# Kernel optimization log

Measured on AMD Instinct MI355X. Metric: run time of the kernel, lower is better.

The kernel has to match this reference:

```python
import jax, jax.numpy as jnp
import numpy as np

DIM = 2048
N_HEADS = 16
HEAD_DIM = DIM // N_HEADS
ROPE_BASE = 10000


def l2norm(x, axis=-1, eps=1e-12):
    n = jnp.sqrt(jnp.sum(x * x, axis=axis, keepdims=True))
    return x / jnp.maximum(n, eps)


def rope_tables(T, dim, base, dtype):
    theta = 1.0 / (base ** (jnp.arange(0, dim, 2, dtype=dtype) / dim))  # [dim/2]
    ang = jnp.arange(T, dtype=dtype)[:, None] * theta[None, :]          # [T, dim/2]
    return jnp.sin(ang), jnp.cos(ang)


def apply_rope(x, sin, cos):
    # x: [B, H, T, D]; sin/cos: [T, D/2] (half-split convention, not interleaved)
    half = x.shape[-1] // 2
    xr, xi = x[..., :half], x[..., half:]
    yr = xr * cos - xi * sin
    yi = xr * sin + xi * cos
    return jnp.concatenate([yr, yi], axis=-1)


def setup_inputs() -> dict:
    key = jax.random.key(0)
    ks = jax.random.split(key, 5)
    B, T = 1, 2048
    x = jax.random.normal(ks[0], (B, T, DIM), dtype=jnp.float32)
    wq = jax.random.normal(ks[1], (DIM, DIM), dtype=jnp.float32) * 0.02
    wk = jax.random.normal(ks[2], (DIM, DIM), dtype=jnp.float32) * 0.02
    wv = jax.random.normal(ks[3], (DIM, DIM), dtype=jnp.float32) * 0.02
    wo = jax.random.normal(ks[4], (DIM, DIM), dtype=jnp.float32) * 0.02
    sqk = jnp.ones((N_HEADS, 1, HEAD_DIM), dtype=jnp.float32) * (1.0 / DIM ** 0.5)
    return {"x": x, "wq": wq, "wk": wk, "wv": wv, "wo": wo, "sqk": sqk}


def reference(x, wq, wk, wv, wo, sqk):
    B, T, C = x.shape
    H, D = N_HEADS, HEAD_DIM
    restore = C ** 0.5  # restore_scale_sqk = sqkinit / sqkscale
    actual_sqk = sqk * restore  # [H, 1, D]

    def proj(w):
        return jnp.einsum('btc,oc->bto', x, w).reshape(B, T, H, D).transpose(0, 2, 1, 3)

    q = proj(wq)  # [B, H, T, D]
    new_k = proj(wk)
    new_v = proj(wv)

    sin, cos = rope_tables(T, D, ROPE_BASE, x.dtype)
    q = apply_rope(q, sin, cos) * actual_sqk
    k = apply_rope(new_k, sin, cos) * actual_sqk

    # NOTE: original uses scale=head_dim**0.5 (multiplies by sqrt(D))
    scores = jnp.einsum('bhqd,bhkd->bhqk', q, k) * (D ** 0.5)
    mask = jnp.tril(jnp.ones((T, T), dtype=bool))
    scores = jnp.where(mask, scores, jnp.finfo(scores.dtype).min)
    attn = jax.nn.softmax(scores, axis=-1)
    out = jnp.einsum('bhqk,bhkd->bhqd', attn, new_v)  # [B, H, T, D]
    out = out.transpose(0, 2, 1, 3).reshape(B, T, C)
    out = jnp.einsum('btc,oc->bto', out, wo)
    return (l2norm(out), (new_k, new_v))
```

## Files before the change

### kernel.cpp

```cpp
#include <hip/hip_runtime.h>

typedef __bf16 bf16x8 __attribute__((ext_vector_type(8)));
typedef float f32x4 __attribute__((ext_vector_type(4)));
typedef unsigned short us4 __attribute__((ext_vector_type(4)));

constexpr int TT = 2048;
constexpr int CC = 2048;
constexpr int HH = 16;
constexpr int DD = 128;

__device__ __forceinline__ unsigned short f2bf(float f) {
  unsigned u = __builtin_bit_cast(unsigned, f);
  u += 0x7FFFu + ((u >> 16) & 1u);
  return (unsigned short)(u >> 16);
}
__device__ __forceinline__ float bf2f(unsigned short b) {
  unsigned u = ((unsigned)b) << 16;
  return __builtin_bit_cast(float, u);
}

__device__ __forceinline__ void gld_lds16(const unsigned short* g, unsigned short* l) {
  __builtin_amdgcn_global_load_lds(
      (const __attribute__((address_space(1))) unsigned int*)g,
      (__attribute__((address_space(3))) unsigned int*)l,
      16, 0, 0);
}

__device__ __forceinline__ int soff(int qt) {
  int g = qt >> 2, rem = qt & 3;
  return (g + 1) * (2 * g + rem);
}

__global__ __launch_bounds__(256) void k_cvt5(
    const float* __restrict__ s0, const float* __restrict__ s1,
    const float* __restrict__ s2, const float* __restrict__ s3,
    const float* __restrict__ s4,
    unsigned short* __restrict__ d0, unsigned short* __restrict__ d1,
    unsigned short* __restrict__ d2, unsigned short* __restrict__ d3,
    unsigned short* __restrict__ d4) {
  const int m = blockIdx.y;
  const float* src = (m == 0) ? s0 : (m == 1) ? s1 : (m == 2) ? s2 : (m == 3) ? s3 : s4;
  unsigned short* dst = (m == 0) ? d0 : (m == 1) ? d1 : (m == 2) ? d2 : (m == 3) ? d3 : d4;
  int i = blockIdx.x * 256 + threadIdx.x;
  const float4* s = (const float4*)src;
  float4 a = s[2 * i], b = s[2 * i + 1];
  us4 lo = { f2bf(a.x), f2bf(a.y), f2bf(a.z), f2bf(a.w) };
  us4 hi = { f2bf(b.x), f2bf(b.y), f2bf(b.z), f2bf(b.w) };
  us4* d = (us4*)dst;
  d[2 * i] = lo;
  d[2 * i + 1] = hi;
}

#define WAIT_LGKM0                                      \
  asm volatile("s_waitcnt lgkmcnt(0)" ::: "memory");    \
  __builtin_amdgcn_sched_barrier(0);
#define BAR __builtin_amdgcn_s_barrier();

__global__ __launch_bounds__(512, 2) void k_gemm192(
    const unsigned short* __restrict__ A, const unsigned short* __restrict__ B,
    unsigned short* __restrict__ qraw,
    float* __restrict__ outk, float* __restrict__ outv) {
  __shared__ alignas(16) unsigned short As[2][256 * 64];
  __shared__ alignas(16) unsigned short Bs[2][192 * 64];
  const int K = CC, NT = K >> 6, NT2 = NT >> 1;
  const int tid = threadIdx.x;
  const int m0 = blockIdx.y * 256, n0 = blockIdx.x * 192;
  const int wid = tid >> 6, lane = tid & 63;
  const int wr = wid >> 2, wc = wid & 3;
  const int lr = lane & 15, lg = lane >> 4;

  auto stA = [&](int buf, int jb, int tile) {
#pragma unroll
    for (int j = jb; j < jb + 2; ++j) {
      const int ch = tid + j * 512;
      const int r = ch >> 3, c8 = ch & 7;
      gld_lds16(A + (size_t)(m0 + r) * K + tile * 64 + ((c8 ^ (r & 7)) * 8),
                &As[buf][ch * 8]);
    }
  };
  auto stB2 = [&](int buf, int tile) {
#pragma unroll
    for (int j = 0; j < 2; ++j) {
      const int ch = tid + j * 512;
      const int r = ch >> 3, c8 = ch & 7;
      gld_lds16(B + (size_t)(n0 + r) * K + tile * 64 + ((c8 ^ (r & 7)) * 8),
                &Bs[buf][ch * 8]);
    }
  };
  auto stB1 = [&](int buf, int tile) {
    const int ch = tid + 1024;
    const int r = ch >> 3, c8 = ch & 7;
    gld_lds16(B + (size_t)(n0 + r) * K + tile * 64 + ((c8 ^ (r & 7)) * 8),
              &Bs[buf][ch * 8]);
  };

  f32x4 acc[8][3] = {};
  bf16x8 alo[4][2], ahi[4][2], b01[2][2], b2v[2];

  auto rdAlo = [&](int d) {
#pragma unroll
    for (int im = 0; im < 4; ++im)
#pragma unroll
      for (int kk = 0; kk < 2; ++kk) {
        const int row = wr * 128 + im * 16 + lr;
        alo[im][kk] = *(const bf16x8*)(&As[d][row * 64 + (((kk * 4 + lg) ^ (row & 7)) * 8)]);
      }
  };
  auto rdAhi = [&](int d) {
#pragma unroll
    for (int im = 0; im < 4; ++im)
#pragma unroll
      for (int kk = 0; kk < 2; ++kk) {
        const int row = wr * 128 + (4 + im) * 16 + lr;
        ahi[im][kk] = *(const bf16x8*)(&As[d][row * 64 + (((kk * 4 + lg) ^ (row & 7)) * 8)]);
      }
  };
  auto rdB01 = [&](int d) {
#pragma unroll
    for (int in = 0; in < 2; ++in)
#pragma unroll
      for (int kk = 0; kk < 2; ++kk) {
        const int row = wc * 48 + in * 16 + lr;
        b01[in][kk] = *(const bf16x8*)(&Bs[d][row * 64 + (((kk * 4 + lg) ^ (row & 7)) * 8)]);
      }
  };
  auto rdB2 = [&](int d) {
#pragma unroll
    for (int kk = 0; kk < 2; ++kk) {
      const int row = wc * 48 + 32 + lr;
      b2v[kk] = *(const bf16x8*)(&Bs[d][row * 64 + (((kk * 4 + lg) ^ (row & 7)) * 8)]);
    }
  };

  auto q_lo01 = [&]() {
    __builtin_amdgcn_s_setprio(1);
#pragma unroll
    for (int im = 0; im < 4; ++im)
#pragma unroll
      for (int in = 0; in < 2; ++in)
#pragma unroll
        for (int kk = 0; kk < 2; ++kk)
          acc[im][in] = __builtin_amdgcn_mfma_f32_16x16x32_bf16(alo[im][kk], b01[in][kk], acc[im][in], 0, 0, 0);
    __builtin_amdgcn_s_setprio(0);
  };
  auto q_lo2 = [&]() {
    __builtin_amdgcn_s_setprio(1);
#pragma unroll
    for (int im = 0; im < 4; ++im)
#pragma unroll
      for (int kk = 0; kk < 2; ++kk)
        acc[im][2] = __builtin_amdgcn_mfma_f32_16x16x32_bf16(alo[im][kk], b2v[kk], acc[im][2], 0, 0, 0);
    __builtin_amdgcn_s_setprio(0);
  };
  auto q_hi2 = [&]() {
    __builtin_amdgcn_s_setprio(1);
#pragma unroll
    for (int im = 0; im < 4; ++im)
#pragma unroll
      for (int kk = 0; kk < 2; ++kk)
        acc[4 + im][2] = __builtin_amdgcn_mfma_f32_16x16x32_bf16(ahi[im][kk], b2v[kk], acc[4 + im][2], 0, 0, 0);
    __builtin_amdgcn_s_setprio(0);
  };
  auto q_hi01 = [&]() {
    __builtin_amdgcn_s_setprio(1);
#pragma unroll
    for (int im = 0; im < 4; ++im)
#pragma unroll
      for (int in = 0; in < 2; ++in)
#pragma unroll
        for (int kk = 0; kk < 2; ++kk)
          acc[4 + im][in] = __builtin_amdgcn_mfma_f32_16x16x32_bf16(ahi[im][kk], b01[in][kk], acc[4 + im][in], 0, 0, 0);
    __builtin_amdgcn_s_setprio(0);
  };

  stB2(0, 0); stB1(0, 0); stA(0, 0, 0); stA(0, 2, 0);
  stB2(1, 1); stB1(1, 1);
  asm volatile("s_waitcnt vmcnt(3)" ::: "memory");
  __builtin_amdgcn_sched_barrier(0);
  BAR

  for (int t = 0; t < NT2; ++t) {
    const int t1 = 2 * t + 1, t2 = 2 * t + 2, t3 = 2 * t + 3;
    const bool s2 = t2 < NT;

    rdAlo(0); rdB01(0);
    stA(1, 0, t1);
    BAR WAIT_LGKM0
    q_lo01();
    BAR
    rdB2(0);
    stA(1, 2, t1);
    BAR WAIT_LGKM0
    q_lo2();
    BAR
    rdAhi(0);
    if (s2) stB2(0, t2);
    BAR WAIT_LGKM0
    q_hi2();
    BAR
    if (s2) stB1(0, t2);
    q_hi01();
    if (s2) { asm volatile("s_waitcnt vmcnt(3)" ::: "memory"); }
    else    { asm volatile("s_waitcnt vmcnt(0)" ::: "memory"); }
    __builtin_amdgcn_sched_barrier(0);
    BAR

    rdAlo(1); rdB01(1);
    if (s2) stA(0, 0, t2);
    BAR WAIT_LGKM0
    q_lo01();
    BAR
    rdB2(1);
    if (s2) stA(0, 2, t2);
    BAR WAIT_LGKM0
    q_lo2();
    BAR
    rdAhi(1);
    if (s2) stB2(1, t3);
    BAR WAIT_LGKM0
    q_hi2();
    BAR
    if (s2) stB1(1, t3);
    q_hi01();
    if (s2) { asm volatile("s_waitcnt vmcnt(3)" ::: "memory"); }
    else    { asm volatile("s_waitcnt vmcnt(0)" ::: "memory"); }
    __builtin_amdgcn_sched_barrier(0);
    BAR
  }

#pragma unroll
  for (int mf = 0; mf < 8; ++mf) {
    const int row = m0 + wr * 128 + mf * 16 + lg * 4;
#pragma unroll
    for (int nf = 0; nf < 3; ++nf) {
      const int col = n0 + wc * 48 + nf * 16 + lr;
#pragma unroll
      for (int r = 0; r < 4; ++r) {
        float v = acc[mf][nf][r];
        int rr = row + r;
        if (col < 2048) {
          qraw[(size_t)rr * 2048 + col] = f2bf(v);
        } else if (col < 4096) {
          int c = col - 2048;
          outk[(size_t)(c >> 7) * (TT * DD) + (size_t)rr * DD + (c & 127)] = v;
        } else {
          int c = col - 4096;
          outv[(size_t)(c >> 7) * (TT * DD) + (size_t)rr * DD + (c & 127)] = v;
        }
      }
    }
  }
}

__global__ __launch_bounds__(512, 2) void k_gemm8p(
    const unsigned short* __restrict__ A, const unsigned short* __restrict__ B,
    int N, int K, int kspan,
    float* __restrict__ out0, float* __restrict__ out1,
    float* __restrict__ out2, float* __restrict__ out3) {
  __shared__ alignas(16) unsigned short As[2][2][128 * 64];
  __shared__ alignas(16) unsigned short Bs[2][2][128 * 64];
  const int tid = threadIdx.x;
  const int m0 = blockIdx.y * 256, n0 = blockIdx.x * 256;
  const int kbeg = blockIdx.z * kspan;
  const int NT = kspan >> 6, NT2 = NT >> 1;
  const int wid = tid >> 6, lane = tid & 63;
  const int wr = wid >> 2, wc = wid & 3;
  const int lr = lane & 15, lg = lane >> 4;
  const int bh = wc >> 1, brow0 = (wc & 1) * 64;

  const int sr0 = tid >> 3, sc0 = tid & 7;
  const unsigned short* Ab = A + kbeg;
  const unsigned short* Bb = B + kbeg;

  auto stageA = [&](int buf, int half, int tile) {
    const int koff = tile * 64;
#pragma unroll
    for (int j = 0; j < 2; ++j) {
      const int r = sr0 + j * 64;
      gld_lds16(Ab + (size_t)(m0 + half * 128 + r) * K + koff + ((sc0 ^ (r & 7)) * 8),
                &As[buf][half][(tid + j * 512) * 8]);
    }
  };
  auto stageB = [&](int buf, int half, int tile) {
    const int koff = tile * 64;
#pragma unroll
    for (int j = 0; j < 2; ++j) {
      const int r = sr0 + j * 64;
      gld_lds16(Bb + (size_t)(n0 + half * 128 + r) * K + koff + ((sc0 ^ (r & 7)) * 8),
                &Bs[buf][half][(tid + j * 512) * 8]);
    }
  };

  f32x4 acc[8][4] = {};
  bf16x8 alo[4][2], ahi[4][2], ba[2][2], bb[2][2];

  auto rdAlo = [&](int d) {
#pragma unroll
    for (int im = 0; im < 4; ++im)
#pragma unroll
      for (int kk = 0; kk < 2; ++kk) {
        const int row = im * 16 + lr;
        alo[im][kk] = *(const bf16x8*)(&As[d][wr][row * 64 + (((kk * 4 + lg) ^ (row & 7)) * 8)]);
      }
  };
  auto rdAhi = [&](int d) {
#pragma unroll
    for (int im = 0; im < 4; ++im)
#pragma unroll
      for (int kk = 0; kk < 2; ++kk) {
        const int row = (4 + im) * 16 + lr;
        ahi[im][kk] = *(const bf16x8*)(&As[d][wr][row * 64 + (((kk * 4 + lg) ^ (row & 7)) * 8)]);
      }
  };
  auto rdBa = [&](int d) {
#pragma unroll
    for (int in = 0; in < 2; ++in)
#pragma unroll
      for (int kk = 0; kk < 2; ++kk) {
        const int row = brow0 + in * 16 + lr;
        ba[in][kk] = *(const bf16x8*)(&Bs[d][bh][row * 64 + (((kk * 4 + lg) ^ (row & 7)) * 8)]);
      }
  };
  auto rdBb = [&](int d) {
#pragma unroll
    for (int in = 0; in < 2; ++in)
#pragma unroll
      for (int kk = 0; kk < 2; ++kk) {
        const int row = brow0 + (2 + in) * 16 + lr;
        bb[in][kk] = *(const bf16x8*)(&Bs[d][bh][row * 64 + (((kk * 4 + lg) ^ (row & 7)) * 8)]);
      }
  };

#define MFMA_Q(MB, NB, AF, BF)                                                     \
  __builtin_amdgcn_s_setprio(1);                                                   \
  _Pragma("unroll") for (int im = 0; im < 4; ++im)                                 \
      _Pragma("unroll") for (int in = 0; in < 2; ++in)                             \
          _Pragma("unroll") for (int kk = 0; kk < 2; ++kk)                         \
              acc[MB + im][NB + in] = __builtin_amdgcn_mfma_f32_16x16x32_bf16(     \
                  AF[im][kk], BF[in][kk], acc[MB + im][NB + in], 0, 0, 0);         \
  __builtin_amdgcn_s_setprio(0);

  stageB(0, 0, 0); stageB(0, 1, 0); stageA(0, 0, 0); stageA(0, 1, 0);
  if (NT > 1) { stageB(1, 0, 1); stageB(1, 1, 1); }
  asm volatile("s_waitcnt vmcnt(4)" ::: "memory");
  __builtin_amdgcn_sched_barrier(0);
  BAR

  for (int t = 0; t < NT2; ++t) {
    const int t1 = 2 * t + 1, t2 = 2 * t + 2, t3 = 2 * t + 3;
    const bool s2 = t2 < NT, s3 = t3 < NT;

    rdAlo(0); rdBa(0);
    stageA(1, 0, t1);
    BAR WAIT_LGKM0
    MFMA_Q(0, 0, alo, ba)
    BAR
    rdBb(0);
    stageA(1, 1, t1);
    BAR WAIT_LGKM0
    MFMA_Q(0, 2, alo, bb)
    BAR
    rdAhi(0);
    if (s2) stageB(0, 0, t2);
    BAR WAIT_LGKM0
    MFMA_Q(4, 2, ahi, bb)
    BAR
    if (s2) stageB(0, 1, t2);
    MFMA_Q(4, 0, ahi, ba)
    if (s2) { asm volatile("s_waitcnt vmcnt(4)" ::: "memory"); }
    else    { asm volatile("s_waitcnt vmcnt(0)" ::: "memory"); }
    __builtin_amdgcn_sched_barrier(0);
    BAR

    rdAlo(1); rdBa(1);
    if (s2) stageA(0, 0, t2);
    BAR WAIT_LGKM0
    MFMA_Q(0, 0, alo, ba)
    BAR
    rdBb(1);
    if (s2) stageA(0, 1, t2);
    BAR WAIT_LGKM0
    MFMA_Q(0, 2, alo, bb)
    BAR
    rdAhi(1);
    if (s3) stageB(1, 0, t3);
    BAR WAIT_LGKM0
    MFMA_Q(4, 2, ahi, bb)
    BAR
    if (s3) stageB(1, 1, t3);
    MFMA_Q(4, 0, ahi, ba)
    if (s3) { asm volatile("s_waitcnt vmcnt(4)" ::: "memory"); }
    else    { asm volatile("s_waitcnt vmcnt(0)" ::: "memory"); }
    __builtin_amdgcn_sched_barrier(0);
    BAR
  }
#undef MFMA_Q

  int z = blockIdx.z;
  float* dst = (z == 0) ? out0 : (z == 1) ? out1 : (z == 2) ? out2 : out3;
#pragma unroll
  for (int mf = 0; mf < 8; ++mf) {
    const int row = m0 + wr * 128 + mf * 16 + lg * 4;
#pragma unroll
    for (int nf = 0; nf < 4; ++nf) {
      const int col = n0 + wc * 64 + nf * 16 + lr;
#pragma unroll
      for (int r = 0; r < 4; ++r) {
        dst[(size_t)(row + r) * N + col] = acc[mf][nf][r];
      }
    }
  }
}
#undef WAIT_LGKM0
#undef BAR

__global__ __launch_bounds__(256) void k_rope(
    const unsigned short* __restrict__ qraw, const float* __restrict__ Kraw,
    const float* __restrict__ sqk,
    unsigned short* __restrict__ qb, unsigned short* __restrict__ kb) {
  const int t = blockIdx.x;
  for (int i = threadIdx.x; i < HH * 64; i += 256) {
    int h = i >> 6, dp = i & 63;
    float theta = expf(-(float)dp * 0.14391156831212787f);
    float ang = (float)t * theta;
    float sn, cs;
    sincosf(ang, &sn, &cs);
    float qr = bf2f(qraw[(size_t)t * CC + h * DD + dp]);
    float qi = bf2f(qraw[(size_t)t * CC + h * DD + dp + 64]);
    const float* kp = Kraw + (size_t)h * TT * DD + (size_t)t * DD;
    float kr = kp[dp], ki = kp[dp + 64];
    float sr = sqk[h * DD + dp];
    float si = sqk[h * DD + dp + 64];
    float qsr = sr * 512.0f, qsi = si * 512.0f;
    float ksr = sr * 45.25483399593904f, ksi = si * 45.25483399593904f;
    unsigned short* qo = qb + ((size_t)h * TT + t) * DD;
    unsigned short* ko = kb + ((size_t)h * TT + t) * DD;
    qo[dp]      = f2bf((qr * cs - qi * sn) * qsr);
    qo[dp + 64] = f2bf((qr * sn + qi * cs) * qsi);
    ko[dp]      = f2bf((kr * cs - ki * sn) * ksr);
    ko[dp + 64] = f2bf((kr * sn + ki * cs) * ksi);
  }
}

__global__ __launch_bounds__(256) void k_vt(
    const float* __restrict__ Vraw, unsigned short* __restrict__ vt) {
  const int h = blockIdx.z;
  const int t0 = blockIdx.x * 64, d0 = blockIdx.y * 64;
  __shared__ unsigned short tile[64][65];
  const float* vp = Vraw + (size_t)h * TT * DD;
  for (int i = threadIdx.x; i < 4096; i += 256) {
    int r = i >> 6, c = i & 63;
    tile[r][c] = f2bf(vp[(size_t)(t0 + r) * DD + d0 + c]);
  }
  __syncthreads();
  unsigned short* op = vt + (size_t)h * DD * TT;
  for (int i = threadIdx.x; i < 4096; i += 256) {
    int dr = i >> 6, tc = i & 63;
    op[(size_t)(d0 + dr) * TT + t0 + tc] = tile[tc][dr];
  }
}

__global__ __launch_bounds__(512) void k_attn_split(
    const unsigned short* __restrict__ qb, const unsigned short* __restrict__ kb,
    const unsigned short* __restrict__ vt,
    unsigned short* __restrict__ po, float* __restrict__ marr, float* __restrict__ larr) {
  const int qt = blockIdx.x, h = blockIdx.y, s = blockIdx.z;
  if (4 * s > qt) return;
  const int slot = h * 40 + soff(qt) + s;
  const int kbeg = 512 * s;
  const int kend = min(kbeg + 512, 128 * qt + 128);
  const int ntiles = (kend - kbeg) >> 6;
  const int tid = threadIdx.x;
  const int wid = tid >> 6, lane = tid & 63;
  const int lr = lane & 15, lg = lane >> 4;
  const int q0 = qt * 128 + wid * 16;

  __shared__ alignas(16) unsigned short Ks[64 * 128];
  __shared__ alignas(16) unsigned short Vs[128 * 64];
  __shared__ alignas(16) unsigned short P[8][16][72];

  const unsigned short* qh = qb + (size_t)h * TT * DD;
  const unsigned short* kh = kb + (size_t)h * TT * DD;
  const unsigned short* vh = vt + (size_t)h * DD * TT;

  bf16x8 qf[4];
#pragma unroll
  for (int c = 0; c < 4; ++c)
    qf[c] = *(const bf16x8*)(qh + (size_t)(q0 + lr) * DD + c * 32 + lg * 8);

  f32x4 acc[8] = {};
  float mrow[4] = {-3e38f, -3e38f, -3e38f, -3e38f};
  float lsum[4] = {0.f, 0.f, 0.f, 0.f};

  for (int kt = 0; kt < ntiles; ++kt) {
    const int k0 = kbeg + kt * 64;
#pragma unroll
    for (int half = 0; half < 2; ++half) {
      int ch = tid + half * 512;
      int r = ch >> 4, c4 = ch & 15;
      gld_lds16(kh + (size_t)(k0 + r) * DD + ((c4 ^ (r & 7)) * 8), Ks + ch * 8);
    }
#pragma unroll
    for (int half = 0; half < 2; ++half) {
      int ch = tid + half * 512;
      int d = ch >> 3, c8 = ch & 7;
      gld_lds16(vh + (size_t)d * TT + k0 + ((c8 ^ (d & 7)) * 8), Vs + ch * 8);
    }
    __syncthreads();

    if (k0 <= q0 + 15) {
      f32x4 sv[4] = {};
#pragma unroll
      for (int ktile = 0; ktile < 4; ++ktile) {
        const int row = ktile * 16 + lr;
#pragma unroll
        for (int c = 0; c < 4; ++c) {
          int chn = (c * 4 + lg) ^ (lr & 7);
          bf16x8 kf = *(const bf16x8*)(Ks + row * 128 + chn * 8);
          sv[ktile] = __builtin_amdgcn_mfma_f32_16x16x32_bf16(qf[c], kf, sv[ktile], 0, 0, 0);
        }
      }
      if (k0 + 63 > q0) {
#pragma unroll
        for (int ktile = 0; ktile < 4; ++ktile)
#pragma unroll
          for (int r = 0; r < 4; ++r) {
            int key = k0 + ktile * 16 + lr;
            int qrow = q0 + lg * 4 + r;
            if (key > qrow) sv[ktile][r] = -1e30f;
          }
      }
      float pmax[4];
#pragma unroll
      for (int r = 0; r < 4; ++r)
        pmax[r] = fmaxf(fmaxf(sv[0][r], sv[1][r]), fmaxf(sv[2][r], sv[3][r]));
#pragma unroll
      for (int msk = 1; msk <= 8; msk <<= 1)
#pragma unroll
        for (int r = 0; r < 4; ++r) pmax[r] = fmaxf(pmax[r], __shfl_xor(pmax[r], msk));
      float p[4][4], ps[4], scl[4];
#pragma unroll
      for (int r = 0; r < 4; ++r) {
        float mn = fmaxf(mrow[r], pmax[r]);
        scl[r] = __expf(mrow[r] - mn);
        mrow[r] = mn;
        ps[r] = 0.f;
#pragma unroll
        for (int ktile = 0; ktile < 4; ++ktile) {
          p[ktile][r] = __expf(sv[ktile][r] - mn);
          ps[r] += p[ktile][r];
        }
      }
#pragma unroll
      for (int msk = 1; msk <= 8; msk <<= 1)
#pragma unroll
        for (int r = 0; r < 4; ++r) ps[r] += __shfl_xor(ps[r], msk);
#pragma unroll
      for (int r = 0; r < 4; ++r) lsum[r] = lsum[r] * scl[r] + ps[r];
#pragma unroll
      for (int n = 0; n < 8; ++n)
#pragma unroll
        for (int r = 0; r < 4; ++r) acc[n][r] *= scl[r];
#pragma unroll
      for (int ktile = 0; ktile < 4; ++ktile)
#pragma unroll
        for (int r = 0; r < 4; ++r)
          P[wid][lg * 4 + r][ktile * 16 + lr] = f2bf(p[ktile][r]);
      asm volatile("s_waitcnt lgkmcnt(0)" ::: "memory");
      __builtin_amdgcn_sched_barrier(0);
      bf16x8 pf[2];
#pragma unroll
      for (int ks = 0; ks < 2; ++ks)
        pf[ks] = *(const bf16x8*)(&P[wid][lr][ks * 32 + lg * 8]);
#pragma unroll
      for (int n = 0; n < 8; ++n) {
        const int row = n * 16 + lr;
#pragma unroll
        for (int ks = 0; ks < 2; ++ks) {
          int chn = (ks * 4 + lg) ^ (lr & 7);
          bf16x8 vf = *(const bf16x8*)(Vs + row * 64 + chn * 8);
          acc[n] = __builtin_amdgcn_mfma_f32_16x16x32_bf16(pf[ks], vf, acc[n], 0, 0, 0);
        }
      }
    }
    __syncthreads();
  }

  unsigned short* pob = po + (size_t)slot * (128 * DD);
#pragma unroll
  for (int n = 0; n < 8; ++n)
#pragma unroll
    for (int r = 0; r < 4; ++r) {
      int row = wid * 16 + lg * 4 + r;
      pob[(size_t)row * DD + n * 16 + lr] = f2bf(acc[n][r]);
    }
  if (lr == 0) {
#pragma unroll
    for (int r = 0; r < 4; ++r) {
      int row = wid * 16 + lg * 4 + r;
      marr[(size_t)slot * 128 + row] = mrow[r];
      larr[(size_t)slot * 128 + row] = lsum[r];
    }
  }
}

__global__ __launch_bounds__(256) void k_attn_reduce(
    const unsigned short* __restrict__ po, const float* __restrict__ marr,
    const float* __restrict__ larr, unsigned short* __restrict__ ob) {
  const int qt = blockIdx.x, h = blockIdx.y;
  const int ns = (qt >> 2) + 1;
  const int sb = h * 40 + soff(qt);
  const int tid = threadIdx.x;
  const int row = tid >> 1, d0 = (tid & 1) * 64;
  float mstar = -3e38f;
  for (int s = 0; s < ns; ++s) mstar = fmaxf(mstar, marr[(size_t)(sb + s) * 128 + row]);
  float w[4];
  float ltot = 0.f;
  for (int s = 0; s < ns; ++s) {
    w[s] = __expf(marr[(size_t)(sb + s) * 128 + row] - mstar);
    ltot += w[s] * larr[(size_t)(sb + s) * 128 + row];
  }
  float inv = 1.0f / ltot;
  float o[64] = {};
  for (int s = 0; s < ns; ++s) {
    const bf16x8* pp = (const bf16x8*)(po + (size_t)(sb + s) * (128 * DD) + (size_t)row * DD + d0);
    float ws = w[s];
#pragma unroll
    for (int j = 0; j < 8; ++j) {
      bf16x8 v = pp[j];
#pragma unroll
      for (int e = 0; e < 8; ++e) o[j * 8 + e] += ws * (float)v[e];
    }
  }
  unsigned short* op = ob + (size_t)(qt * 128 + row) * CC + h * DD + d0;
#pragma unroll
  for (int j = 0; j < 16; ++j) {
    us4 t = { f2bf(o[4 * j] * inv), f2bf(o[4 * j + 1] * inv),
              f2bf(o[4 * j + 2] * inv), f2bf(o[4 * j + 3] * inv) };
    ((us4*)op)[j] = t;
  }
}

__global__ __launch_bounds__(256) void k_l2norm(
    const float* __restrict__ Of0, const float* __restrict__ Of1,
    const float* __restrict__ Of2, const float* __restrict__ Of3,
    float* __restrict__ out) {
  const int t = blockIdx.x;
  const int tid = threadIdx.x;
  const float4* p0 = (const float4*)(Of0 + (size_t)t * CC);
  const float4* p1 = (const float4*)(Of1 + (size_t)t * CC);
  const float4* p2 = (const float4*)(Of2 + (size_t)t * CC);
  const float4* p3 = (const float4*)(Of3 + (size_t)t * CC);
  float4 a = p0[2 * tid], b = p0[2 * tid + 1];
  float4 a1 = p1[2 * tid], b1 = p1[2 * tid + 1];
  float4 a2 = p2[2 * tid], b2 = p2[2 * tid + 1];
  float4 a3 = p3[2 * tid], b3 = p3[2 * tid + 1];
  a.x += a1.x + a2.x + a3.x; a.y += a1.y + a2.y + a3.y;
  a.z += a1.z + a2.z + a3.z; a.w += a1.w + a2.w + a3.w;
  b.x += b1.x + b2.x + b3.x; b.y += b1.y + b2.y + b3.y;
  b.z += b1.z + b2.z + b3.z; b.w += b1.w + b2.w + b3.w;
  float ss = a.x * a.x + a.y * a.y + a.z * a.z + a.w * a.w +
             b.x * b.x + b.y * b.y + b.z * b.z + b.w * b.w;
#pragma unroll
  for (int msk = 1; msk < 64; msk <<= 1) ss += __shfl_xor(ss, msk);
  __shared__ float red[4];
  if ((tid & 63) == 0) red[tid >> 6] = ss;
  __syncthreads();
  ss = red[0] + red[1] + red[2] + red[3];
  float sc = 1.0f / fmaxf(sqrtf(ss), 1e-12f);
  float4 oa = { a.x * sc, a.y * sc, a.z * sc, a.w * sc };
  float4 obv = { b.x * sc, b.y * sc, b.z * sc, b.w * sc };
  float4* o = (float4*)(out + (size_t)t * CC);
  o[2 * tid] = oa;
  o[2 * tid + 1] = obv;
}

extern "C" void kernel_launch(void* const* d_in, const int* in_sizes, int n_in,
                              void* d_out, int out_size, void* d_ws, size_t ws_size,
                              hipStream_t stream) {
  const float* x   = (const float*)d_in[0];
  const float* wq  = (const float*)d_in[1];
  const float* wk  = (const float*)d_in[2];
  const float* wv  = (const float*)d_in[3];
  const float* wo  = (const float*)d_in[4];
  const float* sqk = (const float*)d_in[5];

  float* out_norm = (float*)d_out;
  float* out_k = out_norm + (size_t)4 * 1024 * 1024;
  float* out_v = out_norm + (size_t)8 * 1024 * 1024;

  char* ws = (char*)d_ws;
  unsigned short* xb  = (unsigned short*)(ws);
  unsigned short* w1b = (unsigned short*)(ws + (8u << 20));
  unsigned short* wob = (unsigned short*)(ws + (32u << 20));
  unsigned short* qb  = (unsigned short*)(ws + (40u << 20));
  unsigned short* kb  = (unsigned short*)(ws + (48u << 20));
  unsigned short* vtb = (unsigned short*)(ws + (56u << 20));
  unsigned short* obb = (unsigned short*)(ws + (64u << 20));
  unsigned short* qraw = (unsigned short*)(ws + (72u << 20));

  unsigned short* po = (unsigned short*)(ws);
  float* marr = (float*)(ws + (22u << 20));
  float* larr = (float*)(ws + (23u << 20));

  float* Of0 = (float*)(ws + (72u << 20));
  float* Of1 = (float*)(ws);
  float* Of2 = (float*)(ws + (16u << 20));
  float* Of3 = (float*)(ws + (40u << 20));

  k_cvt5<<<dim3(2048, 5), 256, 0, stream>>>(
      x, wq, wk, wv, wo,
      xb, w1b, w1b + (size_t)4 * 1024 * 1024, w1b + (size_t)8 * 1024 * 1024, wob);

  k_gemm192<<<dim3(32, 8), 512, 0, stream>>>(xb, w1b, qraw, out_k, out_v);

  k_rope<<<TT, 256, 0, stream>>>(qraw, out_k, sqk, qb, kb);
  k_vt<<<dim3(32, 2, 16), 256, 0, stream>>>(out_v, vtb);

  k_attn_split<<<dim3(16, 16, 4), 512, 0, stream>>>(qb, kb, vtb, po, marr, larr);
  k_attn_reduce<<<dim3(16, 16), 256, 0, stream>>>(po, marr, larr, obb);

  k_gemm8p<<<dim3(8, 8, 4), 512, 0, stream>>>(obb, wob, CC, CC, CC / 4,
                                              Of0, Of1, Of2, Of3);

  k_l2norm<<<TT, 256, 0, stream>>>(Of0, Of1, Of2, Of3, out_norm);
}
```

Baseline: 216.6 us.

## Replace split-K attention and reduce with paired causal tiles and double-buffered KV

Drops the split-KV attention kernel and its separate reduction pass. Each block now handles two 64-row query tiles from opposite ends of the causal triangle (gA and 31-gA), so every block does the same amount of work. K and V tiles are double-buffered in LDS so the next tile loads while the current one is computed, and the output is normalised and written straight to the final layout. This removes the partial-output writes, the extra kernel launch and the reduce pass, but cuts the grid to 256 blocks, which lowers parallelism, and doubles LDS use per block.

```diff
diff --git a/kernel.cpp b/kernel.cpp
--- a/kernel.cpp
+++ b/kernel.cpp
@@ -24,11 +24,6 @@
       (const __attribute__((address_space(1))) unsigned int*)g,
       (__attribute__((address_space(3))) unsigned int*)l,
       16, 0, 0);
-}
-
-__device__ __forceinline__ int soff(int qt) {
-  int g = qt >> 2, rem = qt & 3;
-  return (g + 1) * (2 * g + rem);
 }
 
 __global__ __launch_bounds__(256) void k_cvt5(
@@ -460,29 +455,42 @@
   }
 }
 
-__global__ __launch_bounds__(512) void k_attn_split(
+__global__ __launch_bounds__(512) void k_attn_pair(
     const unsigned short* __restrict__ qb, const unsigned short* __restrict__ kb,
-    const unsigned short* __restrict__ vt,
-    unsigned short* __restrict__ po, float* __restrict__ marr, float* __restrict__ larr) {
-  const int qt = blockIdx.x, h = blockIdx.y, s = blockIdx.z;
-  if (4 * s > qt) return;
-  const int slot = h * 40 + soff(qt) + s;
-  const int kbeg = 512 * s;
-  const int kend = min(kbeg + 512, 128 * qt + 128);
-  const int ntiles = (kend - kbeg) >> 6;
+    const unsigned short* __restrict__ vt, unsigned short* __restrict__ ob) {
+  const int gA = blockIdx.x, h = blockIdx.y;
+  const int gB = 31 - gA;
+  const int ntiles = gB + 1;
   const int tid = threadIdx.x;
   const int wid = tid >> 6, lane = tid & 63;
   const int lr = lane & 15, lg = lane >> 4;
-  const int q0 = qt * 128 + wid * 16;
-
-  __shared__ alignas(16) unsigned short Ks[64 * 128];
-  __shared__ alignas(16) unsigned short Vs[128 * 64];
+  const int gq = (wid >> 2) ? gB : gA;
+  const int q0 = gq * 64 + (wid & 3) * 16;
+
+  __shared__ alignas(16) unsigned short Ks[2][64 * 128];
+  __shared__ alignas(16) unsigned short Vs[2][128 * 64];
   __shared__ alignas(16) unsigned short P[8][16][72];
 
   const unsigned short* qh = qb + (size_t)h * TT * DD;
   const unsigned short* kh = kb + (size_t)h * TT * DD;
   const unsigned short* vh = vt + (size_t)h * DD * TT;
 
+  auto stageKV = [&](int buf, int kt) {
+    const int k0 = kt * 64;
+#pragma unroll
+    for (int half = 0; half < 2; ++half) {
+      int ch = tid + half * 512;
+      int r = ch >> 4, c4 = ch & 15;
+      gld_lds16(kh + (size_t)(k0 + r) * DD + ((c4 ^ (r & 7)) * 8), Ks[buf] + ch * 8);
+    }
+#pragma unroll
+    for (int half = 0; half < 2; ++half) {
+      int ch = tid + half * 512;
+      int d = ch >> 3, c8 = ch & 7;
+      gld_lds16(vh + (size_t)d * TT + k0 + ((c8 ^ (d & 7)) * 8), Vs[buf] + ch * 8);
+    }
+  };
+
   bf16x8 qf[4];
 #pragma unroll
   for (int c = 0; c < 4; ++c)
@@ -492,21 +500,15 @@
   float mrow[4] = {-3e38f, -3e38f, -3e38f, -3e38f};
   float lsum[4] = {0.f, 0.f, 0.f, 0.f};
 
+  stageKV(0, 0);
+  asm volatile("s_waitcnt vmcnt(0)" ::: "memory");
+  __builtin_amdgcn_sched_barrier(0);
+  __builtin_amdgcn_s_barrier();
+
   for (int kt = 0; kt < ntiles; ++kt) {
-    const int k0 = kbeg + kt * 64;
-#pragma unroll
-    for (int half = 0; half < 2; ++half) {
-      int ch = tid + half * 512;
-      int r = ch >> 4, c4 = ch & 15;
-      gld_lds16(kh + (size_t)(k0 + r) * DD + ((c4 ^ (r & 7)) * 8), Ks + ch * 8);
-    }
-#pragma unroll
-    for (int half = 0; half < 2; ++half) {
-      int ch = tid + half * 512;
-      int d = ch >> 3, c8 = ch & 7;
-      gld_lds16(vh + (size_t)d * TT + k0 + ((c8 ^ (d & 7)) * 8), Vs + ch * 8);
-    }
-    __syncthreads();
+    const int cur = kt & 1;
+    const int k0 = kt * 64;
+    if (kt + 1 < ntiles) stageKV(cur ^ 1, kt + 1);
 
     if (k0 <= q0 + 15) {
       f32x4 sv[4] = {};
@@ -516,7 +518,7 @@
 #pragma unroll
         for (int c = 0; c < 4; ++c) {
           int chn = (c * 4 + lg) ^ (lr & 7);
-          bf16x8 kf = *(const bf16x8*)(Ks + row * 128 + chn * 8);
+          bf16x8 kf = *(const bf16x8*)(Ks[cur] + row * 128 + chn * 8);
           sv[ktile] = __builtin_amdgcn_mfma_f32_16x16x32_bf16(qf[c], kf, sv[ktile], 0, 0, 0);
         }
       }
@@ -578,67 +580,26 @@
 #pragma unroll
         for (int ks = 0; ks < 2; ++ks) {
           int chn = (ks * 4 + lg) ^ (lr & 7);
-          bf16x8 vf = *(const bf16x8*)(Vs + row * 64 + chn * 8);
+          bf16x8 vf = *(const bf16x8*)(Vs[cur] + row * 64 + chn * 8);
           acc[n] = __builtin_amdgcn_mfma_f32_16x16x32_bf16(pf[ks], vf, acc[n], 0, 0, 0);
         }
       }
     }
-    __syncthreads();
-  }
-
-  unsigned short* pob = po + (size_t)slot * (128 * DD);
+    asm volatile("s_waitcnt vmcnt(0)" ::: "memory");
+    __builtin_amdgcn_sched_barrier(0);
+    __builtin_amdgcn_s_barrier();
+  }
+
+  float inv[4];
+#pragma unroll
+  for (int r = 0; r < 4; ++r) inv[r] = 1.0f / lsum[r];
 #pragma unroll
   for (int n = 0; n < 8; ++n)
 #pragma unroll
     for (int r = 0; r < 4; ++r) {
-      int row = wid * 16 + lg * 4 + r;
-      pob[(size_t)row * DD + n * 16 + lr] = f2bf(acc[n][r]);
-    }
-  if (lr == 0) {
-#pragma unroll
-    for (int r = 0; r < 4; ++r) {
-      int row = wid * 16 + lg * 4 + r;
-      marr[(size_t)slot * 128 + row] = mrow[r];
-      larr[(size_t)slot * 128 + row] = lsum[r];
-    }
-  }
-}
-
-__global__ __launch_bounds__(256) void k_attn_reduce(
-    const unsigned short* __restrict__ po, const float* __restrict__ marr,
-    const float* __restrict__ larr, unsigned short* __restrict__ ob) {
-  const int qt = blockIdx.x, h = blockIdx.y;
-  const int ns = (qt >> 2) + 1;
-  const int sb = h * 40 + soff(qt);
-  const int tid = threadIdx.x;
-  const int row = tid >> 1, d0 = (tid & 1) * 64;
-  float mstar = -3e38f;
-  for (int s = 0; s < ns; ++s) mstar = fmaxf(mstar, marr[(size_t)(sb + s) * 128 + row]);
-  float w[4];
-  float ltot = 0.f;
-  for (int s = 0; s < ns; ++s) {
-    w[s] = __expf(marr[(size_t)(sb + s) * 128 + row] - mstar);
-    ltot += w[s] * larr[(size_t)(sb + s) * 128 + row];
-  }
-  float inv = 1.0f / ltot;
-  float o[64] = {};
-  for (int s = 0; s < ns; ++s) {
-    const bf16x8* pp = (const bf16x8*)(po + (size_t)(sb + s) * (128 * DD) + (size_t)row * DD + d0);
-    float ws = w[s];
-#pragma unroll
-    for (int j = 0; j < 8; ++j) {
-      bf16x8 v = pp[j];
-#pragma unroll
-      for (int e = 0; e < 8; ++e) o[j * 8 + e] += ws * (float)v[e];
-    }
-  }
-  unsigned short* op = ob + (size_t)(qt * 128 + row) * CC + h * DD + d0;
-#pragma unroll
-  for (int j = 0; j < 16; ++j) {
-    us4 t = { f2bf(o[4 * j] * inv), f2bf(o[4 * j + 1] * inv),
-              f2bf(o[4 * j + 2] * inv), f2bf(o[4 * j + 3] * inv) };
-    ((us4*)op)[j] = t;
-  }
+      int t = q0 + lg * 4 + r;
+      ob[(size_t)t * CC + h * DD + n * 16 + lr] = f2bf(acc[n][r] * inv[r]);
+    }
 }
 
 __global__ __launch_bounds__(256) void k_l2norm(
@@ -699,10 +660,6 @@
   unsigned short* obb = (unsigned short*)(ws + (64u << 20));
   unsigned short* qraw = (unsigned short*)(ws + (72u << 20));
 
-  unsigned short* po = (unsigned short*)(ws);
-  float* marr = (float*)(ws + (22u << 20));
-  float* larr = (float*)(ws + (23u << 20));
-
   float* Of0 = (float*)(ws + (72u << 20));
   float* Of1 = (float*)(ws);
   float* Of2 = (float*)(ws + (16u << 20));
@@ -717,8 +674,7 @@
   k_rope<<<TT, 256, 0, stream>>>(qraw, out_k, sqk, qb, kb);
   k_vt<<<dim3(32, 2, 16), 256, 0, stream>>>(out_v, vtb);
 
-  k_attn_split<<<dim3(16, 16, 4), 512, 0, stream>>>(qb, kb, vtb, po, marr, larr);
-  k_attn_reduce<<<dim3(16, 16), 256, 0, stream>>>(po, marr, larr, obb);
+  k_attn_pair<<<dim3(16, 16), 512, 0, stream>>>(qb, kb, vtb, obb);
 
   k_gemm8p<<<dim3(8, 8, 4), 512, 0, stream>>>(obb, wob, CC, CC, CC / 4,
                                               Of0, Of1, Of2, Of3);
```

Measured after the change: 201.8 us. 1.07x faster.
